# Kernel tuning notes

Measured on AMD Instinct MI355X. Metric: run time of the kernel, lower is better.

Reference implementation:

```python
import jax, jax.numpy as jnp
import numpy as np

N = 50000        # nodes
E_RAND = 800000  # random edges; self-loops appended (A_hat = A + I)
IN = 512         # in_size
OUT = 64         # out_size per head
H = 8            # num_heads
NEG_SLOPE = 0.01 # torch F.leaky_relu default


def setup_inputs() -> dict:
    key = jax.random.key(0)
    k0, k1, k2, k3, k4, k5 = jax.random.split(key, 6)
    X = jax.random.normal(k0, (N, IN), jnp.float32)
    W = jax.random.normal(k1, (OUT * H, IN), jnp.float32) * (1.0 / np.sqrt(IN))
    b = jnp.zeros((OUT * H,), jnp.float32)
    a_l = jax.random.normal(k2, (1, OUT, H), jnp.float32) * 0.1
    a_r = jax.random.normal(k3, (1, OUT, H), jnp.float32) * 0.1
    # edges: random graph plus self-loops so every row segment is non-empty
    row = jnp.concatenate([jax.random.randint(k4, (E_RAND,), 0, N, jnp.int32),
                           jnp.arange(N, dtype=jnp.int32)])
    col = jnp.concatenate([jax.random.randint(k5, (E_RAND,), 0, N, jnp.int32),
                           jnp.arange(N, dtype=jnp.int32)])
    return {"X": X, "W": W, "b": b, "a_l": a_l, "a_r": a_r, "row": row, "col": col}


def reference(X, W, b, a_l, a_r, row, col):
    # dropout p=0.0 -> identity (eval-mode equivalent)
    Z = (X @ W.T + b).reshape(N, OUT, H)              # [N, OUT, H]
    e_l = jnp.sum(Z * a_l, axis=1)                    # [N, H]
    e_r = jnp.sum(Z * a_r, axis=1)                    # [N, H]
    e = jax.nn.leaky_relu(e_l[row] + e_r[col], NEG_SLOPE)  # [E, H]
    # segment softmax over edges grouped by destination row
    m = jax.ops.segment_max(e, row, num_segments=N)   # [N, H]
    ex = jnp.exp(e - m[row])                          # [E, H]
    denom = jax.ops.segment_sum(ex, row, num_segments=N)  # [N, H]
    a = ex / denom[row]                               # [E, H]
    # bspmm: out[i,:,h] = sum_{e: row[e]=i} a[e,h] * Z[col[e],:,h]
    msg = a[:, None, :] * Z[col]                      # [E, OUT, H]
    out = jax.ops.segment_sum(msg, row, num_segments=N)   # [N, OUT, H]
    return out
```

## Files before the change

kernel.cpp:

```cpp
#include <hip/hip_runtime.h>
#include <hip/hip_fp16.h>

#define IN_F 512
#define OH   512
#define NH   8

typedef _Float16 half_t;
typedef __attribute__((ext_vector_type(8))) _Float16 f16x8;
typedef __attribute__((ext_vector_type(4))) float    f32x4;

#define GLOBAL_AS const __attribute__((address_space(1))) void
#define LDS_AS    __attribute__((address_space(3))) void

__device__ static inline void gload_lds16(const void* g, void* l) {
  __builtin_amdgcn_global_load_lds((GLOBAL_AS*)g, (LDS_AS*)l, 16, 0, 0);
}

__global__ __launch_bounds__(256) void k_prep(const float* __restrict__ W,
                                              half_t* __restrict__ Wh, int nWe,
                                              const int* __restrict__ row,
                                              int* __restrict__ deg, int E,
                                              int nbW) {
  int b = blockIdx.x;
  if (b < nbW) {
    int i = (b * 256 + threadIdx.x) * 8;
    if (i >= nWe) return;
    float4 a = *(const float4*)(W + i);
    float4 c = *(const float4*)(W + i + 4);
    f16x8 h;
    h[0] = (half_t)a.x; h[1] = (half_t)a.y; h[2] = (half_t)a.z; h[3] = (half_t)a.w;
    h[4] = (half_t)c.x; h[5] = (half_t)c.y; h[6] = (half_t)c.z; h[7] = (half_t)c.w;
    *(f16x8*)(Wh + i) = h;
  } else {
    int e = (b - nbW) * 256 + threadIdx.x;
    if (e < E) atomicAdd(&deg[row[e]], 1);
  }
}

__global__ __launch_bounds__(512) void k_gemm16_v7(const float* __restrict__ X,
                                                   const half_t* __restrict__ Wh,
                                                   const float* __restrict__ bias,
                                                   const float* __restrict__ al,
                                                   const float* __restrict__ ar,
                                                   half_t* __restrict__ Zh,
                                                   float* __restrict__ el,
                                                   float* __restrict__ er,
                                                   int N, int nwg) {
  __shared__ float  As[2][128 * 32];
  __shared__ half_t Bs[2][512 * 32];
  const int tid  = threadIdx.x;
  const int lane = tid & 63;
  const int wid  = tid >> 6;
  const int wr = wid >> 2, wc = wid & 3;

  int orig = blockIdx.x;
  int xcd = orig & 7;
  int q = nwg >> 3, r = nwg & 7;
  int start = (xcd < r) ? xcd * (q + 1) : r * (q + 1) + (xcd - r) * q;
  int work = start + (orig >> 3);
  const int n0 = work * 128;

  const int rl = lane & 15;
  const int hi16 = lane >> 4;

  int a_row[2], a_goff[2];
#pragma unroll
  for (int c = 0; c < 2; c++) {
    int off = c * 8192 + wid * 1024 + lane * 16;
    int rrow = off >> 7;
    int sg = (off >> 4) & 7;
    a_row[c]  = rrow;
    a_goff[c] = (sg ^ (rrow & 7)) << 2;
  }
  int b_row[4], b_goff[4];
#pragma unroll
  for (int c = 0; c < 4; c++) {
    int off = c * 8192 + wid * 1024 + lane * 16;
    int jr = off >> 6;
    int g  = (off >> 4) & 3;
    b_row[c]  = jr;
    b_goff[c] = (g ^ ((jr >> 1) & 3)) << 3;
  }

#define STAGE(BUF, KT)                                                          \
  do {                                                                          \
    _Pragma("unroll")                                                           \
    for (int c = 0; c < 2; c++) {                                               \
      int an = n0 + a_row[c]; if (an >= N) an = N - 1;                          \
      const float* g = X + (size_t)an * IN_F + (KT) + a_goff[c];                \
      gload_lds16(g, (char*)&As[BUF][0] + c * 8192 + wid * 1024);               \
    }                                                                           \
    _Pragma("unroll")                                                           \
    for (int c = 0; c < 4; c++) {                                               \
      const half_t* g = Wh + (size_t)b_row[c] * IN_F + (KT) + b_goff[c];        \
      gload_lds16(g, (char*)&Bs[BUF][0] + c * 8192 + wid * 1024);               \
    }                                                                           \
  } while (0)

  f32x4 acc[4][8] = {};

  STAGE(0, 0);

#pragma unroll
  for (int ki = 0; ki < 16; ki++) {
    const int cur = ki & 1;
    if (ki < 15) {
      STAGE(cur ^ 1, (ki + 1) * 32);
      asm volatile("s_waitcnt vmcnt(6)" ::: "memory");
    } else {
      asm volatile("s_waitcnt vmcnt(0)" ::: "memory");
    }
    __builtin_amdgcn_sched_barrier(0);
    __builtin_amdgcn_s_barrier();

    f16x8 af[4], bf[8];
#pragma unroll
    for (int m = 0; m < 4; m++) {
      int rr = wr * 64 + m * 16 + rl;
      int r7 = rr & 7;
      const char* base = (const char*)&As[cur][0] + rr * 128;
      f32x4 lo = *(const f32x4*)(base + (((hi16 * 2) ^ r7) << 4));
      f32x4 hi = *(const f32x4*)(base + (((hi16 * 2 + 1) ^ r7) << 4));
      f16x8 a;
#pragma unroll
      for (int u = 0; u < 4; u++) { a[u] = (half_t)lo[u]; a[u + 4] = (half_t)hi[u]; }
      af[m] = a;
    }
#pragma unroll
    for (int n = 0; n < 8; n++) {
      int jr = wc * 128 + n * 16 + rl;
      bf[n] = *(const f16x8*)((const char*)&Bs[cur][0] + jr * 64 +
                              ((hi16 ^ ((jr >> 1) & 3)) << 4));
    }
#pragma unroll
    for (int m = 0; m < 4; m++)
#pragma unroll
      for (int n = 0; n < 8; n++)
        acc[m][n] = __builtin_amdgcn_mfma_f32_16x16x32_f16(af[m], bf[n], acc[m][n], 0, 0, 0);

    __builtin_amdgcn_s_barrier();
  }
#undef STAGE

  float bv[8], av[8], rv[8];
#pragma unroll
  for (int n = 0; n < 8; n++) {
    int j = wc * 128 + n * 16 + rl;
    bv[n] = bias[j]; av[n] = al[j]; rv[n] = ar[j];
  }

  float partl[4][4], partr[4][4];
#pragma unroll
  for (int m = 0; m < 4; m++)
#pragma unroll
    for (int qq = 0; qq < 4; qq++) { partl[m][qq] = 0.f; partr[m][qq] = 0.f; }

#pragma unroll
  for (int n = 0; n < 8; n++) {
    int j = wc * 128 + n * 16 + rl;
#pragma unroll
    for (int m = 0; m < 4; m++) {
      int rbase = n0 + wr * 64 + m * 16 + hi16 * 4;
#pragma unroll
      for (int qq = 0; qq < 4; qq++) {
        float v = acc[m][n][qq] + bv[n];
        int nrow = rbase + qq;
        if (nrow < N) Zh[(size_t)nrow * OH + j] = (half_t)v;
        partl[m][qq] = fmaf(v, av[n], partl[m][qq]);
        partr[m][qq] = fmaf(v, rv[n], partr[m][qq]);
      }
    }
  }
  const int h = rl & 7;
#pragma unroll
  for (int m = 0; m < 4; m++) {
#pragma unroll
    for (int qq = 0; qq < 4; qq++) {
      float pl = partl[m][qq], pr = partr[m][qq];
      pl += __shfl_xor(pl, 8);
      pr += __shfl_xor(pr, 8);
      if (rl < 8) {
        int nrow = n0 + wr * 64 + m * 16 + hi16 * 4 + qq;
        if (nrow < N) {
          atomicAdd(&el[(size_t)nrow * NH + h], pl);
          atomicAdd(&er[(size_t)nrow * NH + h], pr);
        }
      }
    }
  }
}

#define SCAN_B 1024
__global__ __launch_bounds__(SCAN_B) void k_scan1(const int* __restrict__ deg,
                                                  int* __restrict__ off,
                                                  int* __restrict__ sums, int N) {
  __shared__ int s[SCAN_B];
  int tid = threadIdx.x;
  int g = blockIdx.x * SCAN_B + tid;
  int v = (g < N) ? deg[g] : 0;
  s[tid] = v;
  __syncthreads();
  for (int o = 1; o < SCAN_B; o <<= 1) {
    int t = (tid >= o) ? s[tid - o] : 0;
    __syncthreads();
    s[tid] += t;
    __syncthreads();
  }
  if (g < N) off[g] = s[tid] - v;
  if (tid == SCAN_B - 1) sums[blockIdx.x] = s[tid];
}

__global__ __launch_bounds__(SCAN_B) void k_scan3(int* __restrict__ off,
                                                  int* __restrict__ cursor,
                                                  const int* __restrict__ sums,
                                                  int nb, int N, int E) {
  __shared__ int sboff;
  int tid = threadIdx.x;
  if (tid < 64) {
    int v = (tid < nb && tid < (int)blockIdx.x) ? sums[tid] : 0;
#pragma unroll
    for (int s = 1; s < 64; s <<= 1) v += __shfl_xor(v, s);
    if (tid == 0) sboff = v;
  }
  __syncthreads();
  int g = blockIdx.x * SCAN_B + tid;
  if (g < N) {
    int v = off[g] + sboff;
    off[g] = v;
    cursor[g] = v;
  }
  if (g == 0) off[N] = E;
}

__global__ void k_fill(const int* __restrict__ row, const int* __restrict__ col,
                       int* __restrict__ cursor, int* __restrict__ colS, int E) {
  int e = blockIdx.x * blockDim.x + threadIdx.x;
  if (e < E) {
    int r = row[e];
    int p = atomicAdd(&cursor[r], 1);
    colS[p] = col[e];
  }
}

__global__ __launch_bounds__(256) void k_attagg(const half_t* __restrict__ Zh,
                                                const float* __restrict__ el,
                                                const float* __restrict__ er,
                                                const int* __restrict__ off,
                                                const int* __restrict__ colS,
                                                float* __restrict__ out, int N) {
  __shared__ float wts[4][64][NH];
  __shared__ int   cls[4][64];
  int wid = threadIdx.x >> 6, lane = threadIdx.x & 63;
  int i = blockIdx.x * 4 + wid;
  if (i >= N) return;
  int s = off[i], t = off[i + 1];
  int deg = t - s;

  float eli[8];
  {
    const float4* e4 = (const float4*)(el + (size_t)i * NH);
    float4 a = e4[0], b = e4[1];
    eli[0] = a.x; eli[1] = a.y; eli[2] = a.z; eli[3] = a.w;
    eli[4] = b.x; eli[5] = b.y; eli[6] = b.z; eli[7] = b.w;
  }

  float m[8], ehs[8];
  int csave = 0;
#pragma unroll
  for (int h = 0; h < 8; h++) m[h] = -1e30f;
  for (int p = s + lane; p < t; p += 64) {
    int c = __builtin_nontemporal_load(&colS[p]);
    csave = c;
    const float4* e4 = (const float4*)(er + (size_t)c * NH);
    float4 ea = e4[0], eb = e4[1];
    float ev[8] = {ea.x, ea.y, ea.z, ea.w, eb.x, eb.y, eb.z, eb.w};
#pragma unroll
    for (int h = 0; h < 8; h++) {
      float eh = eli[h] + ev[h];
      eh = (eh > 0.f) ? eh : 0.01f * eh;
      ehs[h] = eh;
      m[h] = fmaxf(m[h], eh);
    }
  }
#pragma unroll
  for (int st = 1; st < 64; st <<= 1)
#pragma unroll
    for (int h = 0; h < 8; h++) m[h] = fmaxf(m[h], __shfl_xor(m[h], st));

  float acc[8], den[8];
#pragma unroll
  for (int h = 0; h < 8; h++) { acc[h] = 0.f; den[h] = 0.f; }

  for (int base = s; base < t; base += 64) {
    int p = base + lane;
    if (p < t) {
      int c;
      float eh[8];
      if (deg <= 64) {
        c = csave;
#pragma unroll
        for (int h = 0; h < 8; h++) eh[h] = ehs[h];
      } else {
        c = __builtin_nontemporal_load(&colS[p]);
        const float4* e4 = (const float4*)(er + (size_t)c * NH);
        float4 ea = e4[0], eb = e4[1];
        float ev[8] = {ea.x, ea.y, ea.z, ea.w, eb.x, eb.y, eb.z, eb.w};
#pragma unroll
        for (int h = 0; h < 8; h++) {
          float e2 = eli[h] + ev[h];
          eh[h] = (e2 > 0.f) ? e2 : 0.01f * e2;
        }
      }
      cls[wid][lane] = c;
#pragma unroll
      for (int h = 0; h < 8; h++) {
        float pr = __expf(eh[h] - m[h]);
        den[h] += pr;
        wts[wid][lane][h] = pr;
      }
    }
    int cnt = t - base; if (cnt > 64) cnt = 64;

    int e = 0;
    for (; e + 4 <= cnt; e += 4) {
      int c0 = cls[wid][e + 0], c1 = cls[wid][e + 1];
      int c2 = cls[wid][e + 2], c3 = cls[wid][e + 3];
      f16x8 z0 = *(const f16x8*)(Zh + (size_t)c0 * OH + lane * 8);
      f16x8 z1 = *(const f16x8*)(Zh + (size_t)c1 * OH + lane * 8);
      f16x8 z2 = *(const f16x8*)(Zh + (size_t)c2 * OH + lane * 8);
      f16x8 z3 = *(const f16x8*)(Zh + (size_t)c3 * OH + lane * 8);
      const float* w0 = &wts[wid][e + 0][0];
      const float* w1 = &wts[wid][e + 1][0];
      const float* w2 = &wts[wid][e + 2][0];
      const float* w3 = &wts[wid][e + 3][0];
#pragma unroll
      for (int h = 0; h < 8; h++) {
        acc[h] = fmaf(w0[h], (float)z0[h], acc[h]);
        acc[h] = fmaf(w1[h], (float)z1[h], acc[h]);
        acc[h] = fmaf(w2[h], (float)z2[h], acc[h]);
        acc[h] = fmaf(w3[h], (float)z3[h], acc[h]);
      }
    }
    for (; e < cnt; e++) {
      int c = cls[wid][e];
      f16x8 z = *(const f16x8*)(Zh + (size_t)c * OH + lane * 8);
      const float* w = &wts[wid][e][0];
#pragma unroll
      for (int h = 0; h < 8; h++) acc[h] = fmaf(w[h], (float)z[h], acc[h]);
    }
  }

#pragma unroll
  for (int st = 1; st < 64; st <<= 1)
#pragma unroll
    for (int h = 0; h < 8; h++) den[h] += __shfl_xor(den[h], st);

  f32x4 o0, o1;
  o0[0] = acc[0] / den[0]; o0[1] = acc[1] / den[1];
  o0[2] = acc[2] / den[2]; o0[3] = acc[3] / den[3];
  o1[0] = acc[4] / den[4]; o1[1] = acc[5] / den[5];
  o1[2] = acc[6] / den[6]; o1[3] = acc[7] / den[7];
  __builtin_nontemporal_store(o0, (f32x4*)(out + (size_t)i * OH + lane * 8));
  __builtin_nontemporal_store(o1, (f32x4*)(out + (size_t)i * OH + lane * 8 + 4));
}

extern "C" void kernel_launch(void* const* d_in, const int* in_sizes, int n_in,
                              void* d_out, int out_size, void* d_ws, size_t ws_size,
                              hipStream_t stream) {
  const float* X    = (const float*)d_in[0];
  const float* W    = (const float*)d_in[1];
  const float* bias = (const float*)d_in[2];
  const float* a_l  = (const float*)d_in[3];
  const float* a_r  = (const float*)d_in[4];
  const int*   row  = (const int*)d_in[5];
  const int*   col  = (const int*)d_in[6];
  float* out = (float*)d_out;

  const int N = in_sizes[0] / IN_F;
  const int E = in_sizes[5];
  const int nWe = OH * IN_F;

  auto align_up = [](size_t v) { return (v + 255) & ~(size_t)255; };
  char* p = (char*)d_ws;
  half_t* Wh    = (half_t*)p; p += align_up((size_t)nWe * 2);
  half_t* Zh    = (half_t*)p; p += align_up((size_t)N * OH * 2);
  float* el     = (float*)p;  p += (size_t)N * NH * 4;
  float* er     = (float*)p;  p += align_up((size_t)N * NH * 4);
  int*   deg    = (int*)p;    p += align_up((size_t)N * 4);
  int*   off    = (int*)p;    p += align_up((size_t)(N + 1) * 4);
  int*   cursor = (int*)p;    p += align_up((size_t)N * 4);
  int*   sums   = (int*)p;    p += align_up((size_t)64 * 4);
  int*   colS   = (int*)p;    p += align_up((size_t)E * 4);
  (void)ws_size; (void)n_in; (void)out_size;

  const int nb = (N + SCAN_B - 1) / SCAN_B;

  hipMemsetAsync(deg, 0, (size_t)N * 4, stream);
  hipMemsetAsync(el, 0, (size_t)2 * N * NH * 4, stream);

  const int nbW = (nWe / 8 + 255) / 256;
  const int nbH = (E + 255) / 256;
  hipLaunchKernelGGL(k_prep, dim3(nbW + nbH), dim3(256), 0, stream,
                     W, Wh, nWe, row, deg, E, nbW);

  const int nwg = (N + 127) / 128;
  hipLaunchKernelGGL(k_gemm16_v7, dim3(nwg), dim3(512), 0, stream,
                     X, Wh, bias, a_l, a_r, Zh, el, er, N, nwg);

  hipLaunchKernelGGL(k_scan1, dim3(nb), dim3(SCAN_B), 0, stream, deg, off, sums, N);
  hipLaunchKernelGGL(k_scan3, dim3(nb), dim3(SCAN_B), 0, stream,
                     off, cursor, sums, nb, N, E);
  hipLaunchKernelGGL(k_fill, dim3((E + 255) / 256), dim3(256), 0, stream,
                     row, col, cursor, colS, E);

  hipLaunchKernelGGL(k_attagg, dim3((N + 3) / 4), dim3(256), 0, stream,
                     Zh, el, er, off, colS, out, N);
}
```

Before: 306.8 us.

## Shrink GEMM row tile to 64 and drop XCD-aware block remapping

The fused projection GEMM now covers 64 rows per workgroup instead of 128. Each of the 8 waves owns a 64-column slice across all 64 rows, so the 2x4 wave grid becomes a 1x8 strip and accumulators drop from 4x8 to 4x4 fragments. The launch bound asks for 4 blocks per CU, aiming to raise occupancy and shrink the tail with twice as many workgroups. The XCD-contiguous block remap is removed, and each block still loads the full 512-column W slice per k-step, so W traffic from LDS and L2 per output row doubles.

Result: slower. 343.4 us (+11.9%).

```diff
diff --git a/kernel.cpp b/kernel.cpp
--- a/kernel.cpp
+++ b/kernel.cpp
@@ -37,41 +37,28 @@
   }
 }
 
-__global__ __launch_bounds__(512) void k_gemm16_v7(const float* __restrict__ X,
-                                                   const half_t* __restrict__ Wh,
-                                                   const float* __restrict__ bias,
-                                                   const float* __restrict__ al,
-                                                   const float* __restrict__ ar,
-                                                   half_t* __restrict__ Zh,
-                                                   float* __restrict__ el,
-                                                   float* __restrict__ er,
-                                                   int N, int nwg) {
-  __shared__ float  As[2][128 * 32];
+__global__ __launch_bounds__(512, 4) void k_gemm16_v11(const float* __restrict__ X,
+                                                       const half_t* __restrict__ Wh,
+                                                       const float* __restrict__ bias,
+                                                       const float* __restrict__ al,
+                                                       const float* __restrict__ ar,
+                                                       half_t* __restrict__ Zh,
+                                                       float* __restrict__ el,
+                                                       float* __restrict__ er,
+                                                       int N) {
+  __shared__ float  As[2][64 * 32];
   __shared__ half_t Bs[2][512 * 32];
   const int tid  = threadIdx.x;
   const int lane = tid & 63;
   const int wid  = tid >> 6;
-  const int wr = wid >> 2, wc = wid & 3;
-
-  int orig = blockIdx.x;
-  int xcd = orig & 7;
-  int q = nwg >> 3, r = nwg & 7;
-  int start = (xcd < r) ? xcd * (q + 1) : r * (q + 1) + (xcd - r) * q;
-  int work = start + (orig >> 3);
-  const int n0 = work * 128;
+
+  const int n0 = blockIdx.x * 64;
 
   const int rl = lane & 15;
   const int hi16 = lane >> 4;
 
-  int a_row[2], a_goff[2];
-#pragma unroll
-  for (int c = 0; c < 2; c++) {
-    int off = c * 8192 + wid * 1024 + lane * 16;
-    int rrow = off >> 7;
-    int sg = (off >> 4) & 7;
-    a_row[c]  = rrow;
-    a_goff[c] = (sg ^ (rrow & 7)) << 2;
-  }
+  const int a_row  = (wid * 1024 + lane * 16) >> 7;
+  const int a_goff = ((lane & 7) ^ (a_row & 7)) << 2;
   int b_row[4], b_goff[4];
 #pragma unroll
   for (int c = 0; c < 4; c++) {
@@ -84,11 +71,10 @@
 
 #define STAGE(BUF, KT)                                                          \
   do {                                                                          \
-    _Pragma("unroll")                                                           \
-    for (int c = 0; c < 2; c++) {                                               \
-      int an = n0 + a_row[c]; if (an >= N) an = N - 1;                          \
-      const float* g = X + (size_t)an * IN_F + (KT) + a_goff[c];                \
-      gload_lds16(g, (char*)&As[BUF][0] + c * 8192 + wid * 1024);               \
+    {                                                                           \
+      int an = n0 + a_row; if (an >= N) an = N - 1;                             \
+      const float* g = X + (size_t)an * IN_F + (KT) + a_goff;                   \
+      gload_lds16(g, (char*)&As[BUF][0] + wid * 1024);                          \
     }                                                                           \
     _Pragma("unroll")                                                           \
     for (int c = 0; c < 4; c++) {                                               \
@@ -97,7 +83,7 @@
     }                                                                           \
   } while (0)
 
-  f32x4 acc[4][8] = {};
+  f32x4 acc[4][4] = {};
 
   STAGE(0, 0);
 
@@ -106,17 +92,17 @@
     const int cur = ki & 1;
     if (ki < 15) {
       STAGE(cur ^ 1, (ki + 1) * 32);
-      asm volatile("s_waitcnt vmcnt(6)" ::: "memory");
+      asm volatile("s_waitcnt vmcnt(5)" ::: "memory");
     } else {
       asm volatile("s_waitcnt vmcnt(0)" ::: "memory");
     }
     __builtin_amdgcn_sched_barrier(0);
     __builtin_amdgcn_s_barrier();
 
-    f16x8 af[4], bf[8];
+    f16x8 af[4], bf[4];
 #pragma unroll
     for (int m = 0; m < 4; m++) {
-      int rr = wr * 64 + m * 16 + rl;
+      int rr = m * 16 + rl;
       int r7 = rr & 7;
       const char* base = (const char*)&As[cur][0] + rr * 128;
       f32x4 lo = *(const f32x4*)(base + (((hi16 * 2) ^ r7) << 4));
@@ -127,25 +113,25 @@
       af[m] = a;
     }
 #pragma unroll
-    for (int n = 0; n < 8; n++) {
-      int jr = wc * 128 + n * 16 + rl;
+    for (int n = 0; n < 4; n++) {
+      int jr = wid * 64 + n * 16 + rl;
       bf[n] = *(const f16x8*)((const char*)&Bs[cur][0] + jr * 64 +
                               ((hi16 ^ ((jr >> 1) & 3)) << 4));
     }
 #pragma unroll
     for (int m = 0; m < 4; m++)
 #pragma unroll
-      for (int n = 0; n < 8; n++)
+      for (int n = 0; n < 4; n++)
         acc[m][n] = __builtin_amdgcn_mfma_f32_16x16x32_f16(af[m], bf[n], acc[m][n], 0, 0, 0);
 
     __builtin_amdgcn_s_barrier();
   }
 #undef STAGE
 
-  float bv[8], av[8], rv[8];
-#pragma unroll
-  for (int n = 0; n < 8; n++) {
-    int j = wc * 128 + n * 16 + rl;
+  float bv[4], av[4], rv[4];
+#pragma unroll
+  for (int n = 0; n < 4; n++) {
+    int j = wid * 64 + n * 16 + rl;
     bv[n] = bias[j]; av[n] = al[j]; rv[n] = ar[j];
   }
 
@@ -156,11 +142,11 @@
     for (int qq = 0; qq < 4; qq++) { partl[m][qq] = 0.f; partr[m][qq] = 0.f; }
 
 #pragma unroll
-  for (int n = 0; n < 8; n++) {
-    int j = wc * 128 + n * 16 + rl;
+  for (int n = 0; n < 4; n++) {
+    int j = wid * 64 + n * 16 + rl;
 #pragma unroll
     for (int m = 0; m < 4; m++) {
-      int rbase = n0 + wr * 64 + m * 16 + hi16 * 4;
+      int rbase = n0 + m * 16 + hi16 * 4;
 #pragma unroll
       for (int qq = 0; qq < 4; qq++) {
         float v = acc[m][n][qq] + bv[n];
@@ -180,7 +166,7 @@
       pl += __shfl_xor(pl, 8);
       pr += __shfl_xor(pr, 8);
       if (rl < 8) {
-        int nrow = n0 + wr * 64 + m * 16 + hi16 * 4 + qq;
+        int nrow = n0 + m * 16 + hi16 * 4 + qq;
         if (nrow < N) {
           atomicAdd(&el[(size_t)nrow * NH + h], pl);
           atomicAdd(&er[(size_t)nrow * NH + h], pr);
@@ -403,9 +389,9 @@
   hipLaunchKernelGGL(k_prep, dim3(nbW + nbH), dim3(256), 0, stream,
                      W, Wh, nWe, row, deg, E, nbW);
 
-  const int nwg = (N + 127) / 128;
-  hipLaunchKernelGGL(k_gemm16_v7, dim3(nwg), dim3(512), 0, stream,
-                     X, Wh, bias, a_l, a_r, Zh, el, er, N, nwg);
+  const int nwg = (N + 63) / 64;
+  hipLaunchKernelGGL(k_gemm16_v11, dim3(nwg), dim3(512), 0, stream,
+                     X, Wh, bias, a_l, a_r, Zh, el, er, N);
 
   hipLaunchKernelGGL(k_scan1, dim3(nb), dim3(SCAN_B), 0, stream, deg, off, sums, N);
   hipLaunchKernelGGL(k_scan3, dim3(nb), dim3(SCAN_B), 0, stream,
```

## Fuse CSR fill into GEMM launch and fold el/er zeroing into prep

Applied to the files above, without the earlier changes.

Moves the edge-scatter (CSR fill) work into extra blocks of the GEMM kernel so the atomic-bound fill overlaps with the matrix multiply, and reorders scans ahead of the GEMM. The el/er memset is folded into the prep kernel as extra blocks. This removes two launches and lets the memory-latency-bound fill run alongside compute. In exchange, the fill blocks now allocate the GEMM's large static LDS, which can limit how many of them run concurrently. The XCD remapping also only applies to the GEMM block range.

Result: faster. 280.1 us, median of 2 (-8.7%).

```diff
diff --git a/kernel.cpp b/kernel.cpp
--- a/kernel.cpp
+++ b/kernel.cpp
@@ -20,7 +20,8 @@
                                               half_t* __restrict__ Wh, int nWe,
                                               const int* __restrict__ row,
                                               int* __restrict__ deg, int E,
-                                              int nbW) {
+                                              float* __restrict__ elr, int nZ4,
+                                              int nbW, int nbH) {
   int b = blockIdx.x;
   if (b < nbW) {
     int i = (b * 256 + threadIdx.x) * 8;
@@ -31,23 +32,41 @@
     h[0] = (half_t)a.x; h[1] = (half_t)a.y; h[2] = (half_t)a.z; h[3] = (half_t)a.w;
     h[4] = (half_t)c.x; h[5] = (half_t)c.y; h[6] = (half_t)c.z; h[7] = (half_t)c.w;
     *(f16x8*)(Wh + i) = h;
-  } else {
+  } else if (b < nbW + nbH) {
     int e = (b - nbW) * 256 + threadIdx.x;
     if (e < E) atomicAdd(&deg[row[e]], 1);
-  }
-}
-
-__global__ __launch_bounds__(512) void k_gemm16_v7(const float* __restrict__ X,
-                                                   const half_t* __restrict__ Wh,
-                                                   const float* __restrict__ bias,
-                                                   const float* __restrict__ al,
-                                                   const float* __restrict__ ar,
-                                                   half_t* __restrict__ Zh,
-                                                   float* __restrict__ el,
-                                                   float* __restrict__ er,
-                                                   int N, int nwg) {
+  } else {
+    int i = (b - nbW - nbH) * 256 + threadIdx.x;
+    if (i < nZ4) ((float4*)elr)[i] = make_float4(0.f, 0.f, 0.f, 0.f);
+  }
+}
+
+__global__ __launch_bounds__(512) void k_mega(const float* __restrict__ X,
+                                              const half_t* __restrict__ Wh,
+                                              const float* __restrict__ bias,
+                                              const float* __restrict__ al,
+                                              const float* __restrict__ ar,
+                                              half_t* __restrict__ Zh,
+                                              float* __restrict__ el,
+                                              float* __restrict__ er,
+                                              int N, int nwgG,
+                                              const int* __restrict__ row,
+                                              const int* __restrict__ col,
+                                              int* __restrict__ cursor,
+                                              int* __restrict__ colS, int E) {
   __shared__ float  As[2][128 * 32];
   __shared__ half_t Bs[2][512 * 32];
+
+  if (blockIdx.x >= nwgG) {
+    int e = (blockIdx.x - nwgG) * 512 + threadIdx.x;
+    if (e < E) {
+      int r = row[e];
+      int p = atomicAdd(&cursor[r], 1);
+      colS[p] = col[e];
+    }
+    return;
+  }
+
   const int tid  = threadIdx.x;
   const int lane = tid & 63;
   const int wid  = tid >> 6;
@@ -55,7 +74,7 @@
 
   int orig = blockIdx.x;
   int xcd = orig & 7;
-  int q = nwg >> 3, r = nwg & 7;
+  int q = nwgG >> 3, r = nwgG & 7;
   int start = (xcd < r) ? xcd * (q + 1) : r * (q + 1) + (xcd - r) * q;
   int work = start + (orig >> 3);
   const int n0 = work * 128;
@@ -232,16 +251,6 @@
   if (g == 0) off[N] = E;
 }
 
-__global__ void k_fill(const int* __restrict__ row, const int* __restrict__ col,
-                       int* __restrict__ cursor, int* __restrict__ colS, int E) {
-  int e = blockIdx.x * blockDim.x + threadIdx.x;
-  if (e < E) {
-    int r = row[e];
-    int p = atomicAdd(&cursor[r], 1);
-    colS[p] = col[e];
-  }
-}
-
 __global__ __launch_bounds__(256) void k_attagg(const half_t* __restrict__ Zh,
                                                 const float* __restrict__ el,
                                                 const float* __restrict__ er,
@@ -396,21 +405,22 @@
   const int nb = (N + SCAN_B - 1) / SCAN_B;
 
   hipMemsetAsync(deg, 0, (size_t)N * 4, stream);
-  hipMemsetAsync(el, 0, (size_t)2 * N * NH * 4, stream);
 
   const int nbW = (nWe / 8 + 255) / 256;
   const int nbH = (E + 255) / 256;
-  hipLaunchKernelGGL(k_prep, dim3(nbW + nbH), dim3(256), 0, stream,
-                     W, Wh, nWe, row, deg, E, nbW);
-
-  const int nwg = (N + 127) / 128;
-  hipLaunchKernelGGL(k_gemm16_v7, dim3(nwg), dim3(512), 0, stream,
-                     X, Wh, bias, a_l, a_r, Zh, el, er, N, nwg);
+  const int nZ4 = 2 * N * NH / 4;
+  const int nbZ = (nZ4 + 255) / 256;
+  hipLaunchKernelGGL(k_prep, dim3(nbW + nbH + nbZ), dim3(256), 0, stream,
+                     W, Wh, nWe, row, deg, E, el, nZ4, nbW, nbH);
 
   hipLaunchKernelGGL(k_scan1, dim3(nb), dim3(SCAN_B), 0, stream, deg, off, sums, N);
   hipLaunchKernelGGL(k_scan3, dim3(nb), dim3(SCAN_B), 0, stream,
                      off, cursor, sums, nb, N, E);
-  hipLaunchKernelGGL(k_fill, dim3((E + 255) / 256), dim3(256), 0, stream,
+
+  const int nwgG = (N + 127) / 128;
+  const int nbF  = (E + 511) / 512;
+  hipLaunchKernelGGL(k_mega, dim3(nwgG + nbF), dim3(512), 0, stream,
+                     X, Wh, bias, a_l, a_r, Zh, el, er, N, nwgG,
                      row, col, cursor, colS, E);
 
   hipLaunchKernelGGL(k_attagg, dim3((N + 3) / 4), dim3(256), 0, stream,
```
